# Kernel tuning notes

Hardware: AMD Instinct MI355X
Metric: run time of the kernel (lower is better)

Reference implementation:

```python
import jax, jax.numpy as jnp
import numpy as np

BN_EPS = 1e-5


def setup_inputs() -> dict:
    key = jax.random.key(0)
    k1, k2, k3, k4 = jax.random.split(key, 4)
    B, C, H, W = 16, 128, 128, 128
    x = jax.random.normal(k1, (B, C, H, W), dtype=jnp.float32)
    gamma = jax.random.normal(k2, (1,), dtype=jnp.float32)
    bn_weight = jax.random.uniform(k3, (C,), dtype=jnp.float32)
    bn_bias = jax.random.normal(k4, (C,), dtype=jnp.float32)
    return {"x": x, "gamma": gamma, "bn_weight": bn_weight, "bn_bias": bn_bias}


def reference(x, gamma, bn_weight, bn_bias):
    B, C, H, W = x.shape
    q = x.reshape(B, C, H * W)                      # proj_query: [B, C, HW]
    # energy[b, i, j] = <channel i, channel j>
    energy = jnp.einsum('bin,bjn->bij', q, q)       # [B, C, C]
    energy_new = jnp.max(energy, axis=-1, keepdims=True) - energy
    attention = jax.nn.softmax(energy_new, axis=-1)  # [B, C, C]
    out = jnp.einsum('bij,bjn->bin', attention, q)  # [B, C, HW]
    out = out.reshape(B, C, H, W)
    out = gamma * out
    # BatchNorm2d in training mode: batch statistics over (B, H, W) per channel
    mean = jnp.mean(out, axis=(0, 2, 3), keepdims=True)
    var = jnp.var(out, axis=(0, 2, 3), keepdims=True)  # biased variance
    out = (out - mean) * jax.lax.rsqrt(var + BN_EPS)
    out = out * bn_weight[None, :, None, None] + bn_bias[None, :, None, None]
    return out + x
```

## Files before the change

kernel.cpp:

```cpp
#include <hip/hip_runtime.h>

#define BB 16
#define CC 128
#define NN 16384
#define BN_EPS 1e-5f

typedef unsigned short u16;
typedef short short8 __attribute__((ext_vector_type(8)));
typedef float floatx4 __attribute__((ext_vector_type(4)));

__device__ inline float b2f(u16 u) {
    union { unsigned int i; float f; } c; c.i = ((unsigned int)u) << 16; return c.f;
}
__device__ inline u16 f2b(float f) {
    union { float f; unsigned int i; } c; c.f = f;
    unsigned int r = c.i + 0x7fffu + ((c.i >> 16) & 1u);
    return (u16)(r >> 16);
}

#define K1_LD 72
__global__ __launch_bounds__(512, 4) void k_gram(const float* __restrict__ x,
                                                 float* __restrict__ energy,
                                                 float* __restrict__ S)
{
    __shared__ u16 th[128 * K1_LD];
    __shared__ u16 tl[128 * K1_LD];
    const int rbid = blockIdx.x;
    const int xcd  = rbid & 7;
    const int li   = rbid >> 3;
    const int b    = xcd * 2 + (li >> 5);
    const int k0   = (li & 31) * 512;
    const int t    = threadIdx.x;
    const int w = t >> 6, lane = t & 63, quad = lane >> 4, colL = lane & 15;
    const int w2 = w >> 1;
    const int chf = w & 1;

    floatx4 acc[2][4];
#pragma unroll
    for (int rt = 0; rt < 2; ++rt)
#pragma unroll
        for (int ct = 0; ct < 4; ++ct) acc[rt][ct] = {0.f, 0.f, 0.f, 0.f};
    float rs[4];
#pragma unroll
    for (int it = 0; it < 4; ++it) rs[it] = 0.f;

    const float* xb = x + (size_t)b * CC * NN;
    const int rrow = t >> 4;
    const int c4   = t & 15;

    float4 v[4];
#pragma unroll
    for (int it = 0; it < 4; ++it)
        v[it] = *(const float4*)(xb + (size_t)(it * 32 + rrow) * NN + k0 + c4 * 4);

    const int arow0 = w2 * 32 + colL;
    for (int s = 0; s < 8; ++s) {
#pragma unroll
        for (int it = 0; it < 4; ++it) {
            const int row = it * 32 + rrow;
            float4 vv = v[it];
            if (s < 7)
                v[it] = *(const float4*)(xb + (size_t)row * NN + k0 + (s + 1) * 64 + c4 * 4);
            u16 h0 = f2b(vv.x), h1 = f2b(vv.y), h2 = f2b(vv.z), h3 = f2b(vv.w);
            uint2 hv, lv;
            hv.x = (unsigned)h0 | ((unsigned)h1 << 16);
            hv.y = (unsigned)h2 | ((unsigned)h3 << 16);
            lv.x = (unsigned)f2b(vv.x - b2f(h0)) | ((unsigned)f2b(vv.y - b2f(h1)) << 16);
            lv.y = (unsigned)f2b(vv.z - b2f(h2)) | ((unsigned)f2b(vv.w - b2f(h3)) << 16);
            *(uint2*)&th[row * K1_LD + c4 * 4] = hv;
            *(uint2*)&tl[row * K1_LD + c4 * 4] = lv;
            rs[it] += (vv.x + vv.y) + (vv.z + vv.w);
        }
        asm volatile("s_waitcnt lgkmcnt(0)" ::: "memory");
        __builtin_amdgcn_s_barrier();

#pragma unroll
        for (int ks2 = 0; ks2 < 2; ++ks2) {
            const int kk = ks2 * 32 + quad * 8;
            short8 a0h = *(const short8*)&th[(arow0)      * K1_LD + kk];
            short8 a0l = *(const short8*)&tl[(arow0)      * K1_LD + kk];
            short8 a1h = *(const short8*)&th[(arow0 + 16) * K1_LD + kk];
            short8 a1l = *(const short8*)&tl[(arow0 + 16) * K1_LD + kk];
#pragma unroll
            for (int ct = 0; ct < 4; ++ct) {
                const int brow = chf * 64 + ct * 16 + colL;
                short8 bh = *(const short8*)&th[brow * K1_LD + kk];
                short8 bl = *(const short8*)&tl[brow * K1_LD + kk];
                acc[0][ct] = __builtin_amdgcn_mfma_f32_16x16x32_bf16(a0h, bh, acc[0][ct], 0, 0, 0);
                acc[1][ct] = __builtin_amdgcn_mfma_f32_16x16x32_bf16(a1h, bh, acc[1][ct], 0, 0, 0);
                acc[0][ct] = __builtin_amdgcn_mfma_f32_16x16x32_bf16(a0l, bh, acc[0][ct], 0, 0, 0);
                acc[1][ct] = __builtin_amdgcn_mfma_f32_16x16x32_bf16(a1l, bh, acc[1][ct], 0, 0, 0);
                acc[0][ct] = __builtin_amdgcn_mfma_f32_16x16x32_bf16(a0h, bl, acc[0][ct], 0, 0, 0);
                acc[1][ct] = __builtin_amdgcn_mfma_f32_16x16x32_bf16(a1h, bl, acc[1][ct], 0, 0, 0);
            }
        }
        asm volatile("s_waitcnt lgkmcnt(0)" ::: "memory");
        __builtin_amdgcn_s_barrier();
    }

    float* eb = energy + b * CC * CC;
#pragma unroll
    for (int rt = 0; rt < 2; ++rt)
#pragma unroll
        for (int ct = 0; ct < 4; ++ct)
#pragma unroll
            for (int r = 0; r < 4; ++r) {
                int row = w2 * 32 + rt * 16 + quad * 4 + r;
                int col = chf * 64 + ct * 16 + colL;
                atomicAdd(&eb[row * CC + col], acc[rt][ct][r]);
            }

#pragma unroll
    for (int it = 0; it < 4; ++it) {
        float ps = rs[it];
#pragma unroll
        for (int off = 8; off > 0; off >>= 1) ps += __shfl_down(ps, off, 16);
        if (c4 == 0) atomicAdd(&S[b * CC + it * 32 + rrow], ps);
    }
}

__global__ __launch_bounds__(256) void k_soft(const float* __restrict__ energy,
                                              const float* __restrict__ S,
                                              u16* __restrict__ attb,
                                              float* __restrict__ meanacc,
                                              float* __restrict__ e2acc)
{
    const int b = blockIdx.x >> 7;
    const int i = blockIdx.x & 127;
    const int t = threadIdx.x;
    __shared__ float att[128];
    __shared__ float red[256];
    const float* E = energy + b * CC * CC;

    float e = (t < 128) ? E[i * CC + t] : 3.0e38f;
    red[t] = e; __syncthreads();
    for (int s2 = 128; s2 > 0; s2 >>= 1) { if (t < s2) red[t] = fminf(red[t], red[t + s2]); __syncthreads(); }
    float emin = red[0]; __syncthreads();

    float a = (t < 128) ? expf(emin - e) : 0.f;
    red[t] = a; __syncthreads();
    for (int s2 = 128; s2 > 0; s2 >>= 1) { if (t < s2) red[t] += red[t + s2]; __syncthreads(); }
    float Z = red[0]; __syncthreads();

    float attf = 0.f;
    if (t < 128) {
        u16 ab = f2b(a / Z);
        attf = b2f(ab);
        attb[((size_t)b * CC + i) * CC + t] = ab;
        att[t] = attf;
    }
    float mp = (t < 128) ? attf * S[b * CC + t] : 0.f;
    red[t] = mp; __syncthreads();
    for (int s2 = 128; s2 > 0; s2 >>= 1) { if (t < s2) red[t] += red[t + s2]; __syncthreads(); }
    if (t == 0) atomicAdd(&meanacc[i], red[0]);
    __syncthreads();

    const int j    = t & 127;
    const int half = t >> 7;
    const float* Ej = E + j * CC + half * 64;
    float inner = 0.f;
#pragma unroll 8
    for (int k = 0; k < 64; ++k) inner += att[half * 64 + k] * Ej[k];
    red[t] = inner; __syncthreads();
    float contrib = (t < 128) ? (red[t] + red[t + 128]) * att[t] : 0.f;
    __syncthreads();
    red[t] = contrib; __syncthreads();
    for (int s2 = 128; s2 > 0; s2 >>= 1) { if (t < s2) red[t] += red[t + s2]; __syncthreads(); }
    if (t == 0) atomicAdd(&e2acc[i], red[0]);
}

#define K3_LD 136
__global__ __launch_bounds__(256, 4) void k_out(const float* __restrict__ x,
                                                const u16* __restrict__ attb,
                                                const float* __restrict__ meanacc,
                                                const float* __restrict__ e2acc,
                                                const float* __restrict__ gamma,
                                                const float* __restrict__ bnw,
                                                const float* __restrict__ bnb,
                                                float* __restrict__ out)
{
    __shared__ u16 qT[128 * K3_LD];
    __shared__ float alpha[128];
    __shared__ float beta[128];
    const int b   = blockIdx.x >> 7;
    const int nn0 = (blockIdx.x & 127) * 128;
    const int t   = threadIdx.x;

    if (t < 128) {
        float g   = gamma[0];
        const float invBN = 1.f / (float)(BB * NN);
        float m   = g * meanacc[t] * invBN;
        float e2  = g * g * e2acc[t] * invBN;
        float var = e2 - m * m;
        float inv = rsqrtf(var + BN_EPS);
        float wv  = bnw[t];
        alpha[t] = g * wv * inv;
        beta[t]  = bnb[t] - m * wv * inv;
    }

    const float* xb = x + (size_t)b * CC * NN + nn0;
    const int n0 = (t & 31) * 4;
#pragma unroll
    for (int rep = 0; rep < 4; ++rep) {
        const int c0 = ((t >> 5) + rep * 8) * 4;
        float4 f0 = *(const float4*)(xb + (size_t)(c0 + 0) * NN + n0);
        float4 f1 = *(const float4*)(xb + (size_t)(c0 + 1) * NN + n0);
        float4 f2 = *(const float4*)(xb + (size_t)(c0 + 2) * NN + n0);
        float4 f3 = *(const float4*)(xb + (size_t)(c0 + 3) * NN + n0);
        const float fx[4] = {f0.x, f1.x, f2.x, f3.x};
        const float fy[4] = {f0.y, f1.y, f2.y, f3.y};
        const float fz[4] = {f0.z, f1.z, f2.z, f3.z};
        const float fw[4] = {f0.w, f1.w, f2.w, f3.w};
        const float* cols[4] = {fx, fy, fz, fw};
#pragma unroll
        for (int jn = 0; jn < 4; ++jn) {
            int n = n0 + jn;
            int g = ((c0 >> 3) + n) & 15;
            uint2 v;
            v.x = (unsigned)f2b(cols[jn][0]) | ((unsigned)f2b(cols[jn][1]) << 16);
            v.y = (unsigned)f2b(cols[jn][2]) | ((unsigned)f2b(cols[jn][3]) << 16);
            *(uint2*)&qT[n * K3_LD + g * 8 + (c0 & 7)] = v;
        }
    }
    __syncthreads();

    const int w = t >> 6, lane = t & 63, quad = lane >> 4, colL = lane & 15;
    const u16* ag = attb + (size_t)b * CC * CC;
    floatx4 acc[8][2];
#pragma unroll
    for (int rt = 0; rt < 8; ++rt) { acc[rt][0] = {0.f,0.f,0.f,0.f}; acc[rt][1] = {0.f,0.f,0.f,0.f}; }

#pragma unroll
    for (int ks = 0; ks < 4; ++ks) {
        const int kk = ks * 32 + quad * 8;
        const int n_a = w * 32 + colL;
        const int n_b = n_a + 16;
        short8 bf0 = *(const short8*)&qT[n_a * K3_LD + ((((kk) >> 3) + n_a) & 15) * 8];
        short8 bf1 = *(const short8*)&qT[n_b * K3_LD + ((((kk) >> 3) + n_b) & 15) * 8];
#pragma unroll
        for (int rt = 0; rt < 8; ++rt) {
            short8 af = *(const short8*)&ag[(rt * 16 + colL) * CC + kk];
            acc[rt][0] = __builtin_amdgcn_mfma_f32_16x16x32_bf16(af, bf0, acc[rt][0], 0, 0, 0);
            acc[rt][1] = __builtin_amdgcn_mfma_f32_16x16x32_bf16(af, bf1, acc[rt][1], 0, 0, 0);
        }
    }

    float* ob = out + (size_t)b * CC * NN + nn0;
#pragma unroll
    for (int rt = 0; rt < 8; ++rt)
#pragma unroll
        for (int ct = 0; ct < 2; ++ct)
#pragma unroll
            for (int r = 0; r < 4; ++r) {
                int chn = rt * 16 + quad * 4 + r;
                int nn  = w * 32 + ct * 16 + colL;
                float v = alpha[chn] * acc[rt][ct][r] + beta[chn]
                        + xb[(size_t)chn * NN + nn];
                ob[(size_t)chn * NN + nn] = v;
            }
}

extern "C" void kernel_launch(void* const* d_in, const int* in_sizes, int n_in,
                              void* d_out, int out_size, void* d_ws, size_t ws_size,
                              hipStream_t stream)
{
    const float* x     = (const float*)d_in[0];
    const float* gamma = (const float*)d_in[1];
    const float* bnw   = (const float*)d_in[2];
    const float* bnb   = (const float*)d_in[3];
    float* out = (float*)d_out;

    char* ws = (char*)d_ws;
    float* energy  = (float*)(ws);
    float* S       = (float*)(ws + 1048576);
    float* meanacc = (float*)(ws + 1056768);
    float* e2acc   = (float*)(ws + 1057280);
    u16*   attb    = (u16*)(ws + 1057792);

    hipMemsetAsync(ws, 0, 1057792, stream);
    hipLaunchKernelGGL(k_gram, dim3(512), dim3(512), 0, stream, x, energy, S);
    hipLaunchKernelGGL(k_soft, dim3(2048), dim3(256), 0, stream, energy, S, attb, meanacc, e2acc);
    hipLaunchKernelGGL(k_out,  dim3(2048), dim3(256), 0, stream, x, attb, meanacc, e2acc, gamma, bnw, bnb, out);
}
```

Measured before the change: 339.3 us.

## Process two column tiles per k_out block with register prefetch of next x tile

```diff
diff --git a/kernel.cpp b/kernel.cpp
--- a/kernel.cpp
+++ b/kernel.cpp
@@ -16,6 +16,11 @@
     union { float f; unsigned int i; } c; c.f = f;
     unsigned int r = c.i + 0x7fffu + ((c.i >> 16) & 1u);
     return (u16)(r >> 16);
+}
+__device__ inline unsigned cvt_pk_bf16(float a, float b) {
+    unsigned r;
+    asm("v_cvt_pk_bf16_f32 %0, %1, %2" : "=v"(r) : "v"(a), "v"(b));
+    return r;
 }
 
 #define K1_LD 72
@@ -170,7 +175,7 @@
 }
 
 #define K3_LD 136
-__global__ __launch_bounds__(256, 4) void k_out(const float* __restrict__ x,
+__global__ __launch_bounds__(256, 3) void k_out(const float* __restrict__ x,
                                                 const u16* __restrict__ attb,
                                                 const float* __restrict__ meanacc,
                                                 const float* __restrict__ e2acc,
@@ -182,9 +187,9 @@
     __shared__ u16 qT[128 * K3_LD];
     __shared__ float alpha[128];
     __shared__ float beta[128];
-    const int b   = blockIdx.x >> 7;
-    const int nn0 = (blockIdx.x & 127) * 128;
-    const int t   = threadIdx.x;
+    const int b    = blockIdx.x >> 6;
+    const int nn00 = (blockIdx.x & 63) * 256;
+    const int t    = threadIdx.x;
 
     if (t < 128) {
         float g   = gamma[0];
@@ -198,66 +203,97 @@
         beta[t]  = bnb[t] - m * wv * inv;
     }
 
-    const float* xb = x + (size_t)b * CC * NN + nn0;
-    const int n0 = (t & 31) * 4;
+    const float* xb0 = x + (size_t)b * CC * NN;
+    const int n0  = (t & 31) * 4;
+    const int c0b = (t >> 5) * 4;
+
+    float4 f[16];
 #pragma unroll
     for (int rep = 0; rep < 4; ++rep) {
-        const int c0 = ((t >> 5) + rep * 8) * 4;
-        float4 f0 = *(const float4*)(xb + (size_t)(c0 + 0) * NN + n0);
-        float4 f1 = *(const float4*)(xb + (size_t)(c0 + 1) * NN + n0);
-        float4 f2 = *(const float4*)(xb + (size_t)(c0 + 2) * NN + n0);
-        float4 f3 = *(const float4*)(xb + (size_t)(c0 + 3) * NN + n0);
-        const float fx[4] = {f0.x, f1.x, f2.x, f3.x};
-        const float fy[4] = {f0.y, f1.y, f2.y, f3.y};
-        const float fz[4] = {f0.z, f1.z, f2.z, f3.z};
-        const float fw[4] = {f0.w, f1.w, f2.w, f3.w};
-        const float* cols[4] = {fx, fy, fz, fw};
-#pragma unroll
-        for (int jn = 0; jn < 4; ++jn) {
-            int n = n0 + jn;
-            int g = ((c0 >> 3) + n) & 15;
-            uint2 v;
-            v.x = (unsigned)f2b(cols[jn][0]) | ((unsigned)f2b(cols[jn][1]) << 16);
-            v.y = (unsigned)f2b(cols[jn][2]) | ((unsigned)f2b(cols[jn][3]) << 16);
-            *(uint2*)&qT[n * K3_LD + g * 8 + (c0 & 7)] = v;
-        }
-    }
-    __syncthreads();
+        const int c0 = c0b + rep * 32;
+#pragma unroll
+        for (int rr = 0; rr < 4; ++rr)
+            f[rep * 4 + rr] = *(const float4*)(xb0 + (size_t)(c0 + rr) * NN + nn00 + n0);
+    }
 
     const int w = t >> 6, lane = t & 63, quad = lane >> 4, colL = lane & 15;
     const u16* ag = attb + (size_t)b * CC * CC;
-    floatx4 acc[8][2];
-#pragma unroll
-    for (int rt = 0; rt < 8; ++rt) { acc[rt][0] = {0.f,0.f,0.f,0.f}; acc[rt][1] = {0.f,0.f,0.f,0.f}; }
-
-#pragma unroll
-    for (int ks = 0; ks < 4; ++ks) {
-        const int kk = ks * 32 + quad * 8;
-        const int n_a = w * 32 + colL;
-        const int n_b = n_a + 16;
-        short8 bf0 = *(const short8*)&qT[n_a * K3_LD + ((((kk) >> 3) + n_a) & 15) * 8];
-        short8 bf1 = *(const short8*)&qT[n_b * K3_LD + ((((kk) >> 3) + n_b) & 15) * 8];
-#pragma unroll
-        for (int rt = 0; rt < 8; ++rt) {
-            short8 af = *(const short8*)&ag[(rt * 16 + colL) * CC + kk];
-            acc[rt][0] = __builtin_amdgcn_mfma_f32_16x16x32_bf16(af, bf0, acc[rt][0], 0, 0, 0);
-            acc[rt][1] = __builtin_amdgcn_mfma_f32_16x16x32_bf16(af, bf1, acc[rt][1], 0, 0, 0);
-        }
-    }
-
-    float* ob = out + (size_t)b * CC * NN + nn0;
-#pragma unroll
-    for (int rt = 0; rt < 8; ++rt)
-#pragma unroll
-        for (int ct = 0; ct < 2; ++ct)
-#pragma unroll
-            for (int r = 0; r < 4; ++r) {
-                int chn = rt * 16 + quad * 4 + r;
-                int nn  = w * 32 + ct * 16 + colL;
-                float v = alpha[chn] * acc[rt][ct][r] + beta[chn]
-                        + xb[(size_t)chn * NN + nn];
-                ob[(size_t)chn * NN + nn] = v;
+
+#define STAGE_WRITE()                                                          \
+    {                                                                          \
+        _Pragma("unroll")                                                      \
+        for (int rep = 0; rep < 4; ++rep) {                                    \
+            const int c0 = c0b + rep * 32;                                     \
+            float4 f0 = f[rep*4+0], f1 = f[rep*4+1], f2 = f[rep*4+2], f3 = f[rep*4+3]; \
+            uint2 v0, v1, v2, v3;                                              \
+            v0.x = cvt_pk_bf16(f0.x, f1.x); v0.y = cvt_pk_bf16(f2.x, f3.x);    \
+            v1.x = cvt_pk_bf16(f0.y, f1.y); v1.y = cvt_pk_bf16(f2.y, f3.y);    \
+            v2.x = cvt_pk_bf16(f0.z, f1.z); v2.y = cvt_pk_bf16(f2.z, f3.z);    \
+            v3.x = cvt_pk_bf16(f0.w, f1.w); v3.y = cvt_pk_bf16(f2.w, f3.w);    \
+            const int g0 = ((c0 >> 3) + n0) & 15;                              \
+            *(uint2*)&qT[(n0 + 0) * K3_LD + ((g0 + 0) & 15) * 8 + (c0 & 7)] = v0; \
+            *(uint2*)&qT[(n0 + 1) * K3_LD + ((g0 + 1) & 15) * 8 + (c0 & 7)] = v1; \
+            *(uint2*)&qT[(n0 + 2) * K3_LD + ((g0 + 2) & 15) * 8 + (c0 & 7)] = v2; \
+            *(uint2*)&qT[(n0 + 3) * K3_LD + ((g0 + 3) & 15) * 8 + (c0 & 7)] = v3; \
+        }                                                                      \
+    }
+
+    STAGE_WRITE();
+    asm volatile("s_waitcnt lgkmcnt(0)" ::: "memory");
+    __builtin_amdgcn_s_barrier();
+
+    for (int ch = 0; ch < 2; ++ch) {
+        const int nn0 = nn00 + ch * 128;
+        if (ch == 0) {
+#pragma unroll
+            for (int rep = 0; rep < 4; ++rep) {
+                const int c0 = c0b + rep * 32;
+#pragma unroll
+                for (int rr = 0; rr < 4; ++rr)
+                    f[rep * 4 + rr] = *(const float4*)(xb0 + (size_t)(c0 + rr) * NN + nn00 + 128 + n0);
             }
+        }
+
+        floatx4 acc[8][2];
+#pragma unroll
+        for (int rt = 0; rt < 8; ++rt) { acc[rt][0] = {0.f,0.f,0.f,0.f}; acc[rt][1] = {0.f,0.f,0.f,0.f}; }
+
+#pragma unroll
+        for (int ks = 0; ks < 4; ++ks) {
+            const int kk = ks * 32 + quad * 8;
+            const int n_a = w * 32 + colL;
+            const int n_b = n_a + 16;
+            short8 bf0 = *(const short8*)&qT[n_a * K3_LD + (((kk >> 3) + n_a) & 15) * 8];
+            short8 bf1 = *(const short8*)&qT[n_b * K3_LD + (((kk >> 3) + n_b) & 15) * 8];
+#pragma unroll
+            for (int rt = 0; rt < 8; ++rt) {
+                short8 af = *(const short8*)&ag[(rt * 16 + colL) * CC + kk];
+                acc[rt][0] = __builtin_amdgcn_mfma_f32_16x16x32_bf16(af, bf0, acc[rt][0], 0, 0, 0);
+                acc[rt][1] = __builtin_amdgcn_mfma_f32_16x16x32_bf16(af, bf1, acc[rt][1], 0, 0, 0);
+            }
+        }
+
+        const float* xr = xb0 + nn0;
+        float* ob = out + (size_t)b * CC * NN + nn0;
+#pragma unroll
+        for (int rt = 0; rt < 8; ++rt)
+#pragma unroll
+            for (int ct = 0; ct < 2; ++ct)
+#pragma unroll
+                for (int r = 0; r < 4; ++r) {
+                    int chn = rt * 16 + quad * 4 + r;
+                    int nn  = w * 32 + ct * 16 + colL;
+                    ob[(size_t)chn * NN + nn] = alpha[chn] * acc[rt][ct][r] + beta[chn]
+                                              + xr[(size_t)chn * NN + nn];
+                }
+
+        if (ch == 0) {
+            __builtin_amdgcn_s_barrier();
+            STAGE_WRITE();
+            asm volatile("s_waitcnt lgkmcnt(0)" ::: "memory");
+            __builtin_amdgcn_s_barrier();
+        }
+    }
 }
 
 extern "C" void kernel_launch(void* const* d_in, const int* in_sizes, int n_in,
@@ -278,7 +314,7 @@
     u16*   attb    = (u16*)(ws + 1057792);
 
     hipMemsetAsync(ws, 0, 1057792, stream);
-    hipLaunchKernelGGL(k_gram, dim3(512), dim3(512), 0, stream, x, energy, S);
+    hipLaunchKernelGGL(k_gram, dim3(512),  dim3(512), 0, stream, x, energy, S);
     hipLaunchKernelGGL(k_soft, dim3(2048), dim3(256), 0, stream, energy, S, attb, meanacc, e2acc);
-    hipLaunchKernelGGL(k_out,  dim3(2048), dim3(256), 0, stream, x, attb, meanacc, e2acc, gamma, bnw, bnb, out);
-}
+    hipLaunchKernelGGL(k_out,  dim3(1024), dim3(256), 0, stream, x, attb, meanacc, e2acc, gamma, bnw, bnb, out);
+}
```

After: 550.7 us. 62.3% more time.
